# Kernel optimization log

Hardware: AMD Instinct MI355X
Metric: run time of the kernel (lower is better)

Reference implementation:

```python
import jax, jax.numpy as jnp
import numpy as np

N = 50000    # total nodes
F = 32       # raw feature dim
DEG = 32     # padded neighbors per node per relation
B = 2048     # batch nodes
R = 3        # relations


def setup_inputs() -> dict:
    key = jax.random.key(0)
    ks = jax.random.split(key, 12)
    return {
        "nodes": jax.random.randint(ks[0], (B,), 0, N, dtype=jnp.int32),
        "feat_data": jax.random.normal(ks[1], (N, F), dtype=jnp.float32),
        "adj": jax.random.randint(ks[2], (R, N, DEG), 0, N, dtype=jnp.int32),
        "prior": jax.random.uniform(ks[3], (2,), minval=0.1, maxval=0.9, dtype=jnp.float32),
        "w_mlp": jax.random.normal(ks[4], (F, 64), dtype=jnp.float32) * 0.1,
        "b_mlp": jnp.zeros((64,), jnp.float32),
        "alpha1": jax.random.normal(ks[5], (128, R), dtype=jnp.float32) * 0.1,
        "alpha2": jax.random.normal(ks[6], (256, R), dtype=jnp.float32) * 0.1,
        "w_d2": jax.random.normal(ks[7], (448, 2), dtype=jnp.float32) * 0.05,
        "b_d2": jnp.zeros((2,), jnp.float32),
        "w_d1": jax.random.normal(ks[8], (2, 1), dtype=jnp.float32) * 0.5,
        "b_d1": jnp.zeros((1,), jnp.float32),
    }


def _inter_agg(h_all, adj, nodes, alpha, embed_dim):
    """One InterAgg layer. h_all: (N, D) previous-layer features for all nodes;
    adj: (R, N, deg) neighbor ids; nodes: (B,) batch ids; alpha: (2E, R).
    Returns (B, D + 2E)."""
    emb = h_all[:, -embed_dim:]                      # (N, E) last-E slice as in original
    self_full = jnp.take(h_all, nodes, axis=0)       # (B, D)
    self_emb = self_full[:, -embed_dim:]             # (B, E)
    feats = []
    for r in range(R):  # small fixed relation count
        neigh = jnp.take(adj[r], nodes, axis=0)      # (B, deg)
        gathered = jnp.take(emb, neigh.reshape(-1), axis=0)
        agg = gathered.reshape(neigh.shape[0], neigh.shape[1], embed_dim).mean(axis=1)  # masked-mean
        feats.append(jnp.concatenate([agg, self_emb - agg], axis=1))  # IntraAgg concat
    stack = jnp.stack(feats)                         # (R, B, 2E)
    W = jax.nn.softmax(alpha, axis=1)                # (2E, R)
    inter = jnp.einsum('rbe,er->be', stack, W)       # weighted relation combine
    return jnp.concatenate([self_full, inter], axis=1)


def reference(nodes, feat_data, adj, prior, w_mlp, b_mlp, alpha1, alpha2, w_d2, b_d2, w_d1, b_d1):
    # MLP over all nodes (union set == all nodes; per-node values identical)
    h0 = jax.nn.relu(feat_data @ w_mlp + b_mlp)      # (N, 64)
    all_nodes = jnp.arange(h0.shape[0], dtype=jnp.int32)
    h1 = _inter_agg(h0, adj, all_nodes, alpha1, 64)  # (N, 192)
    h2 = _inter_agg(h1, adj, nodes, alpha2, 128)     # (B, 448)
    x = h2 @ w_d2 + b_d2                             # Dense(2)
    x = jax.nn.leaky_relu(x, negative_slope=0.3)
    x = x + jnp.log(prior)
    return jax.nn.sigmoid(x @ w_d1 + b_d1)           # (B, 1)
```

## Files before the change

### kernel.cpp

```cpp
#include <hip/hip_runtime.h>
#include <hip/hip_fp16.h>
#include <math.h>

#define N_NODES 50000
#define F_IN 32
#define DEG 32
#define BATCH 2048
#define NB_STRIDE 100

typedef int int4v __attribute__((ext_vector_type(4)));
typedef unsigned int uint2v __attribute__((ext_vector_type(2)));
typedef float f32x2 __attribute__((ext_vector_type(2)));

__device__ __forceinline__ void softmax3(float a0, float a1, float a2,
                                         float& w0, float& w1, float& w2) {
    float m = fmaxf(a0, fmaxf(a1, a2));
    float e0 = __expf(a0 - m), e1 = __expf(a1 - m), e2 = __expf(a2 - m);
    float s = 1.f / (e0 + e1 + e2);
    w0 = e0 * s; w1 = e1 * s; w2 = e2 * s;
}

__device__ __forceinline__ f32x2 shfl_xor_f2(f32x2 v, int m) {
    v.x = __shfl_xor(v.x, m, 64);
    v.y = __shfl_xor(v.y, m, 64);
    return v;
}

__global__ __launch_bounds__(256) void mlp_kernel(
        const float* __restrict__ feat,
        const float* __restrict__ w,
        const float* __restrict__ b,
        const float* __restrict__ alpha1,
        const float* __restrict__ alpha2,
        float* __restrict__ sw1,
        float* __restrict__ sw2,
        unsigned char* __restrict__ h0q) {
    __shared__ float wl[F_IN * 64];
    __shared__ float fl[8 * F_IN];
    int tid = threadIdx.x;
    if (blockIdx.x == 0) {
        for (int q = tid; q < 384; q += 256) {
            const float* src = (q < 128) ? (alpha1 + q * 3) : (alpha2 + (q - 128) * 3);
            float* dst = (q < 128) ? (sw1 + q * 3) : (sw2 + (q - 128) * 3);
            float w0, w1, w2;
            softmax3(src[0], src[1], src[2], w0, w1, w2);
            dst[0] = w0; dst[1] = w1; dst[2] = w2;
        }
    }
    for (int i = tid; i < F_IN * 64; i += 256) wl[i] = w[i];
    int local = tid >> 5;
    int f2 = (tid & 31) * 2;
    float b0 = b[f2], b1 = b[f2 + 1];
    const int noct = N_NODES / 8;
    for (int q = blockIdx.x; q < noct; q += gridDim.x) {
        int n0 = q * 8;
        __syncthreads();
        fl[tid] = __builtin_nontemporal_load(feat + (size_t)n0 * F_IN + tid);
        __syncthreads();
        float a0 = b0, a1 = b1;
#pragma unroll
        for (int k = 0; k < F_IN; ++k) {
            float v = fl[local * F_IN + k];
            a0 = fmaf(v, wl[k * 64 + f2], a0);
            a1 = fmaf(v, wl[k * 64 + f2 + 1], a1);
        }
        a0 = fmaxf(a0, 0.f);
        a1 = fmaxf(a1, 0.f);
        int n = n0 + local;
        unsigned pk = __builtin_amdgcn_cvt_pk_fp8_f32(a0, a1, 0u, false);
        *reinterpret_cast<unsigned short*>(h0q + (size_t)n * 64 + f2) =
            (unsigned short)pk;
    }
}

__global__ __launch_bounds__(128) void layer1_kernel(
        const int* __restrict__ adj,
        const unsigned char* __restrict__ h0q,
        const float* __restrict__ sw1,
        unsigned char* __restrict__ i1q) {
    __shared__ int nb[16 * NB_STRIDE];
    __shared__ float swl[384];
    int tid = threadIdx.x;
    int n0 = blockIdx.x * 16;
    if (tid < 96)
        reinterpret_cast<float4*>(swl)[tid] = reinterpret_cast<const float4*>(sw1)[tid];
#pragma unroll
    for (int q = tid; q < 384; q += 128) {
        int r = q >> 7;
        int idx = q & 127;
        int m = idx >> 3;
        int d4 = (idx & 7) * 4;
        int4v v = __builtin_nontemporal_load(reinterpret_cast<const int4v*>(
                adj + ((size_t)r * N_NODES + (n0 + m)) * DEG + d4));
        *reinterpret_cast<int4v*>(&nb[m * NB_STRIDE + r * 32 + d4]) = v;
    }
    __syncthreads();
    int w = tid >> 6, j = tid & 63;
    int m = w * 8 + (j >> 3);
    int e = j & 7;
    int n = n0 + m;
    const int* nbrow = nb + m * NB_STRIDE;
    const unsigned char* qb = h0q + 8 * e;
    f32x2 acc0[4] = {}, acc1[4] = {}, acc2[4] = {};
#pragma unroll 8
    for (int t = 0; t < 32; ++t) {
        uint2v d = *reinterpret_cast<const uint2v*>(qb + (size_t)((unsigned)nbrow[t] * 64u));
        acc0[0] += __builtin_amdgcn_cvt_pk_f32_fp8(d.x, false);
        acc0[1] += __builtin_amdgcn_cvt_pk_f32_fp8(d.x, true);
        acc0[2] += __builtin_amdgcn_cvt_pk_f32_fp8(d.y, false);
        acc0[3] += __builtin_amdgcn_cvt_pk_f32_fp8(d.y, true);
    }
#pragma unroll 8
    for (int t = 32; t < 64; ++t) {
        uint2v d = *reinterpret_cast<const uint2v*>(qb + (size_t)((unsigned)nbrow[t] * 64u));
        acc1[0] += __builtin_amdgcn_cvt_pk_f32_fp8(d.x, false);
        acc1[1] += __builtin_amdgcn_cvt_pk_f32_fp8(d.x, true);
        acc1[2] += __builtin_amdgcn_cvt_pk_f32_fp8(d.y, false);
        acc1[3] += __builtin_amdgcn_cvt_pk_f32_fp8(d.y, true);
    }
#pragma unroll 8
    for (int t = 64; t < 96; ++t) {
        uint2v d = *reinterpret_cast<const uint2v*>(qb + (size_t)((unsigned)nbrow[t] * 64u));
        acc2[0] += __builtin_amdgcn_cvt_pk_f32_fp8(d.x, false);
        acc2[1] += __builtin_amdgcn_cvt_pk_f32_fp8(d.x, true);
        acc2[2] += __builtin_amdgcn_cvt_pk_f32_fp8(d.y, false);
        acc2[3] += __builtin_amdgcn_cvt_pk_f32_fp8(d.y, true);
    }

    float sarr[8];
    {
        uint2v sd = *reinterpret_cast<const uint2v*>(qb + (size_t)((unsigned)n * 64u));
        f32x2 s0 = __builtin_amdgcn_cvt_pk_f32_fp8(sd.x, false);
        f32x2 s1 = __builtin_amdgcn_cvt_pk_f32_fp8(sd.x, true);
        f32x2 s2 = __builtin_amdgcn_cvt_pk_f32_fp8(sd.y, false);
        f32x2 s3 = __builtin_amdgcn_cvt_pk_f32_fp8(sd.y, true);
        sarr[0] = s0.x; sarr[1] = s0.y; sarr[2] = s1.x; sarr[3] = s1.y;
        sarr[4] = s2.x; sarr[5] = s2.y; sarr[6] = s3.x; sarr[7] = s3.y;
    }
    float wA[24], wB[24];
    {
        const float4* pa = reinterpret_cast<const float4*>(swl + 24 * e);
        const float4* pb = reinterpret_cast<const float4*>(swl + 192 + 24 * e);
#pragma unroll
        for (int q = 0; q < 6; ++q) {
            float4 ta = pa[q], tb = pb[q];
            wA[4 * q] = ta.x; wA[4 * q + 1] = ta.y; wA[4 * q + 2] = ta.z; wA[4 * q + 3] = ta.w;
            wB[4 * q] = tb.x; wB[4 * q + 1] = tb.y; wB[4 * q + 2] = tb.z; wB[4 * q + 3] = tb.w;
        }
    }
    const float inv = 1.f / 32.f;
    float oa[8], ob[8];
#pragma unroll
    for (int i = 0; i < 8; ++i) {
        float a0 = acc0[i >> 1][i & 1] * inv;
        float a1 = acc1[i >> 1][i & 1] * inv;
        float a2 = acc2[i >> 1][i & 1] * inv;
        float s = sarr[i];
        oa[i] = wA[3 * i] * a0 + wA[3 * i + 1] * a1 + wA[3 * i + 2] * a2;
        ob[i] = wB[3 * i] * (s - a0) + wB[3 * i + 1] * (s - a1) + wB[3 * i + 2] * (s - a2);
    }
    unsigned qa0 = __builtin_amdgcn_cvt_pk_fp8_f32(oa[0], oa[1], 0u, false);
    qa0 = __builtin_amdgcn_cvt_pk_fp8_f32(oa[2], oa[3], qa0, true);
    unsigned qa1 = __builtin_amdgcn_cvt_pk_fp8_f32(oa[4], oa[5], 0u, false);
    qa1 = __builtin_amdgcn_cvt_pk_fp8_f32(oa[6], oa[7], qa1, true);
    uint2v ua = {qa0, qa1};
    __builtin_nontemporal_store(ua,
        reinterpret_cast<uint2v*>(i1q + (size_t)n * 128 + 8 * e));
    unsigned qb0 = __builtin_amdgcn_cvt_pk_fp8_f32(ob[0], ob[1], 0u, false);
    qb0 = __builtin_amdgcn_cvt_pk_fp8_f32(ob[2], ob[3], qb0, true);
    unsigned qb1 = __builtin_amdgcn_cvt_pk_fp8_f32(ob[4], ob[5], 0u, false);
    qb1 = __builtin_amdgcn_cvt_pk_fp8_f32(ob[6], ob[7], qb1, true);
    uint2v ub = {qb0, qb1};
    __builtin_nontemporal_store(ub,
        reinterpret_cast<uint2v*>(i1q + (size_t)n * 128 + 64 + 8 * e));
}

__global__ __launch_bounds__(256) void layer2_kernel(
        const int* __restrict__ nodes,
        const int* __restrict__ adj,
        const unsigned char* __restrict__ h0q,
        const unsigned char* __restrict__ i1q,
        const float* __restrict__ sw2,
        const float* __restrict__ w_d2,
        const float* __restrict__ b_d2,
        const float* __restrict__ w_d1,
        const float* __restrict__ b_d1,
        const float* __restrict__ prior,
        float* __restrict__ out) {
    __shared__ int nb[4][96];
    __shared__ int nid[4];
    __shared__ float swl[768];
    int tid = threadIdx.x;
    int b0 = blockIdx.x * 4;
    if (tid < 4) nid[tid] = nodes[b0 + tid];
    if (tid >= 64 && tid < 256) {
        int q = tid - 64;
        reinterpret_cast<float4*>(swl)[q] = reinterpret_cast<const float4*>(sw2)[q];
    }
    __syncthreads();
    if (tid < 96) {
        int local = tid / 24, rem = tid - local * 24;
        int r = rem >> 3, d4 = (rem & 7) * 4;
        int4v v = __builtin_nontemporal_load(reinterpret_cast<const int4v*>(
                adj + ((size_t)r * N_NODES + nid[local]) * DEG + d4));
        *reinterpret_cast<int4v*>(&nb[local][r * 32 + d4]) = v;
    }
    __syncthreads();
    int local = tid >> 6, j = tid & 63;
    int bb = b0 + local;
    int n = nid[local];
    int g = j >> 4, e = j & 15;
    int idxs[24];
#pragma unroll
    for (int t = 0; t < 24; ++t) idxs[t] = nb[local][t * 4 + g];
    const unsigned char* qbase = i1q + 8 * e;
    f32x2 acc0[4] = {}, acc1[4] = {}, acc2[4] = {};
#pragma unroll
    for (int t = 0; t < 8; ++t) {
        uint2v d = *reinterpret_cast<const uint2v*>(
            qbase + (size_t)((unsigned)idxs[t] * 128u));
        acc0[0] += __builtin_amdgcn_cvt_pk_f32_fp8(d.x, false);
        acc0[1] += __builtin_amdgcn_cvt_pk_f32_fp8(d.x, true);
        acc0[2] += __builtin_amdgcn_cvt_pk_f32_fp8(d.y, false);
        acc0[3] += __builtin_amdgcn_cvt_pk_f32_fp8(d.y, true);
    }
#pragma unroll
    for (int t = 8; t < 16; ++t) {
        uint2v d = *reinterpret_cast<const uint2v*>(
            qbase + (size_t)((unsigned)idxs[t] * 128u));
        acc1[0] += __builtin_amdgcn_cvt_pk_f32_fp8(d.x, false);
        acc1[1] += __builtin_amdgcn_cvt_pk_f32_fp8(d.x, true);
        acc1[2] += __builtin_amdgcn_cvt_pk_f32_fp8(d.y, false);
        acc1[3] += __builtin_amdgcn_cvt_pk_f32_fp8(d.y, true);
    }
#pragma unroll
    for (int t = 16; t < 24; ++t) {
        uint2v d = *reinterpret_cast<const uint2v*>(
            qbase + (size_t)((unsigned)idxs[t] * 128u));
        acc2[0] += __builtin_amdgcn_cvt_pk_f32_fp8(d.x, false);
        acc2[1] += __builtin_amdgcn_cvt_pk_f32_fp8(d.x, true);
        acc2[2] += __builtin_amdgcn_cvt_pk_f32_fp8(d.y, false);
        acc2[3] += __builtin_amdgcn_cvt_pk_f32_fp8(d.y, true);
    }
#pragma unroll
    for (int mm = 16; mm <= 32; mm <<= 1) {
#pragma unroll
        for (int q = 0; q < 4; ++q) {
            acc0[q] += shfl_xor_f2(acc0[q], mm);
            acc1[q] += shfl_xor_f2(acc1[q], mm);
            acc2[q] += shfl_xor_f2(acc2[q], mm);
        }
    }
    const float inv = 1.f / 32.f;
    float p0 = 0.f, p1 = 0.f;
    if (g == 0) {
        float sarr[8];
        {
            uint2v sd = *reinterpret_cast<const uint2v*>(
                qbase + (size_t)((unsigned)n * 128u));
            f32x2 s0 = __builtin_amdgcn_cvt_pk_f32_fp8(sd.x, false);
            f32x2 s1 = __builtin_amdgcn_cvt_pk_f32_fp8(sd.x, true);
            f32x2 s2 = __builtin_amdgcn_cvt_pk_f32_fp8(sd.y, false);
            f32x2 s3 = __builtin_amdgcn_cvt_pk_f32_fp8(sd.y, true);
            sarr[0] = s0.x; sarr[1] = s0.y; sarr[2] = s1.x; sarr[3] = s1.y;
            sarr[4] = s2.x; sarr[5] = s2.y; sarr[6] = s3.x; sarr[7] = s3.y;
        }
        const float* wa = swl + 24 * e;
        const float* wb = swl + 384 + 24 * e;
#pragma unroll
        for (int i = 0; i < 8; ++i) {
            int f = 8 * e + i;
            float a0 = acc0[i >> 1][i & 1] * inv;
            float a1 = acc1[i >> 1][i & 1] * inv;
            float a2 = acc2[i >> 1][i & 1] * inv;
            float s = sarr[i];
            float i2a = wa[3 * i] * a0 + wa[3 * i + 1] * a1 + wa[3 * i + 2] * a2;
            float i2b = wb[3 * i] * (s - a0) + wb[3 * i + 1] * (s - a1) +
                        wb[3 * i + 2] * (s - a2);
            p0 += i2a * w_d2[(192 + f) * 2 + 0] + i2b * w_d2[(320 + f) * 2 + 0];
            p1 += i2a * w_d2[(192 + f) * 2 + 1] + i2b * w_d2[(320 + f) * 2 + 1];
        }
    } else if (g == 1) {
        unsigned d = *reinterpret_cast<const unsigned*>(h0q + (size_t)n * 64 + 4 * e);
        f32x2 lo = __builtin_amdgcn_cvt_pk_f32_fp8(d, false);
        f32x2 hi = __builtin_amdgcn_cvt_pk_f32_fp8(d, true);
        float sv[4] = {lo.x, lo.y, hi.x, hi.y};
#pragma unroll
        for (int i = 0; i < 4; ++i) {
            int f = 4 * e + i;
            p0 += sv[i] * w_d2[f * 2 + 0];
            p1 += sv[i] * w_d2[f * 2 + 1];
        }
    } else if (g == 2) {
        float sarr[8];
        {
            uint2v sd = *reinterpret_cast<const uint2v*>(
                qbase + (size_t)((unsigned)n * 128u));
            f32x2 s0 = __builtin_amdgcn_cvt_pk_f32_fp8(sd.x, false);
            f32x2 s1 = __builtin_amdgcn_cvt_pk_f32_fp8(sd.x, true);
            f32x2 s2 = __builtin_amdgcn_cvt_pk_f32_fp8(sd.y, false);
            f32x2 s3 = __builtin_amdgcn_cvt_pk_f32_fp8(sd.y, true);
            sarr[0] = s0.x; sarr[1] = s0.y; sarr[2] = s1.x; sarr[3] = s1.y;
            sarr[4] = s2.x; sarr[5] = s2.y; sarr[6] = s3.x; sarr[7] = s3.y;
        }
#pragma unroll
        for (int i = 0; i < 8; ++i) {
            int f = 8 * e + i;
            p0 += sarr[i] * w_d2[(64 + f) * 2 + 0];
            p1 += sarr[i] * w_d2[(64 + f) * 2 + 1];
        }
    }
#pragma unroll
    for (int mm = 1; mm <= 32; mm <<= 1) {
        p0 += __shfl_xor(p0, mm, 64);
        p1 += __shfl_xor(p1, mm, 64);
    }
    if (j == 0) {
        float x0 = p0 + b_d2[0], x1 = p1 + b_d2[1];
        x0 = x0 > 0.f ? x0 : 0.3f * x0;
        x1 = x1 > 0.f ? x1 : 0.3f * x1;
        x0 += __logf(prior[0]);
        x1 += __logf(prior[1]);
        float z = x0 * w_d1[0] + x1 * w_d1[1] + b_d1[0];
        out[bb] = 1.f / (1.f + __expf(-z));
    }
}

extern "C" void kernel_launch(void* const* d_in, const int* in_sizes, int n_in,
                              void* d_out, int out_size, void* d_ws, size_t ws_size,
                              hipStream_t stream) {
    const int*   nodes  = (const int*)d_in[0];
    const float* feat   = (const float*)d_in[1];
    const int*   adj    = (const int*)d_in[2];
    const float* prior  = (const float*)d_in[3];
    const float* w_mlp  = (const float*)d_in[4];
    const float* b_mlp  = (const float*)d_in[5];
    const float* alpha1 = (const float*)d_in[6];
    const float* alpha2 = (const float*)d_in[7];
    const float* w_d2   = (const float*)d_in[8];
    const float* b_d2   = (const float*)d_in[9];
    const float* w_d1   = (const float*)d_in[10];
    const float* b_d1   = (const float*)d_in[11];
    float* out = (float*)d_out;

    float* sw1 = (float*)d_ws;
    float* sw2 = sw1 + 128 * 3;
    unsigned char* h0q = (unsigned char*)((char*)d_ws + 8192);
    unsigned char* i1q = h0q + (size_t)N_NODES * 64;

    mlp_kernel<<<2048, 256, 0, stream>>>(feat, w_mlp, b_mlp, alpha1, alpha2,
                                         sw1, sw2, h0q);
    layer1_kernel<<<N_NODES / 16, 128, 0, stream>>>(adj, h0q, sw1, i1q);
    layer2_kernel<<<BATCH / 4, 256, 0, stream>>>(nodes, adj, h0q, i1q, sw2,
                                                 w_d2, b_d2, w_d1, b_d1, prior, out);
}
```

Measured before the change: 55.26 us.

## Split layer1 neighbor loop across 4 lanes with 16-byte gathers and shuffle reduce

Layer1 now runs 256 threads per block. Each node's 64-dim fp8 row is covered by 4 lanes doing 16-byte loads, and the 32 neighbors per relation are split across 4 lane groups whose partial sums are combined with xor shuffles. The relation weights are stored transposed in shared memory so they can be read as float4 vectors. The aim is more memory-level parallelism and wider loads in the gather-bound step, at the cost of extra shuffles and more registers for the accumulators.

```diff
diff --git a/kernel.cpp b/kernel.cpp
--- a/kernel.cpp
+++ b/kernel.cpp
@@ -10,7 +10,9 @@
 
 typedef int int4v __attribute__((ext_vector_type(4)));
 typedef unsigned int uint2v __attribute__((ext_vector_type(2)));
+typedef unsigned int uint4v __attribute__((ext_vector_type(4)));
 typedef float f32x2 __attribute__((ext_vector_type(2)));
+typedef float f32x4 __attribute__((ext_vector_type(4)));
 
 __device__ __forceinline__ void softmax3(float a0, float a1, float a2,
                                          float& w0, float& w1, float& w2) {
@@ -73,21 +75,22 @@
     }
 }
 
-__global__ __launch_bounds__(128) void layer1_kernel(
+__global__ __launch_bounds__(256) void layer1_kernel(
         const int* __restrict__ adj,
         const unsigned char* __restrict__ h0q,
         const float* __restrict__ sw1,
         unsigned char* __restrict__ i1q) {
     __shared__ int nb[16 * NB_STRIDE];
-    __shared__ float swl[384];
+    __shared__ alignas(16) float swlT[6][64];
     int tid = threadIdx.x;
     int n0 = blockIdx.x * 16;
-    if (tid < 96)
-        reinterpret_cast<float4*>(swl)[tid] = reinterpret_cast<const float4*>(sw1)[tid];
-#pragma unroll
-    for (int q = tid; q < 384; q += 128) {
-        int r = q >> 7;
-        int idx = q & 127;
+    for (int t = tid; t < 384; t += 256) {
+        int p = t >> 6, f = t & 63;
+        swlT[p][f] = (p < 3) ? sw1[f * 3 + p] : sw1[(64 + f) * 3 + (p - 3)];
+    }
+    for (int t = tid; t < 384; t += 256) {
+        int r = t >> 7;
+        int idx = t & 127;
         int m = idx >> 3;
         int d4 = (idx & 7) * 4;
         int4v v = __builtin_nontemporal_load(reinterpret_cast<const int4v*>(
@@ -96,83 +99,104 @@
     }
     __syncthreads();
     int w = tid >> 6, j = tid & 63;
-    int m = w * 8 + (j >> 3);
-    int e = j & 7;
-    int n = n0 + m;
-    const int* nbrow = nb + m * NB_STRIDE;
-    const unsigned char* qb = h0q + 8 * e;
-    f32x2 acc0[4] = {}, acc1[4] = {}, acc2[4] = {};
-#pragma unroll 8
-    for (int t = 0; t < 32; ++t) {
-        uint2v d = *reinterpret_cast<const uint2v*>(qb + (size_t)((unsigned)nbrow[t] * 64u));
+    int m = j >> 4;
+    int q = j & 3;
+    int rg = (j >> 2) & 3;
+    int nodeLocal = w * 4 + m;
+    int n = n0 + nodeLocal;
+    const int* nbrow = nb + nodeLocal * NB_STRIDE;
+    const unsigned char* qb = h0q + 16 * q;
+    f32x2 acc0[8] = {}, acc1[8] = {}, acc2[8] = {};
+#pragma unroll
+    for (int t = 0; t < 8; ++t) {
+        unsigned row = (unsigned)nbrow[rg + 4 * t];
+        uint4v d = *reinterpret_cast<const uint4v*>(qb + (size_t)(row * 64u));
         acc0[0] += __builtin_amdgcn_cvt_pk_f32_fp8(d.x, false);
         acc0[1] += __builtin_amdgcn_cvt_pk_f32_fp8(d.x, true);
         acc0[2] += __builtin_amdgcn_cvt_pk_f32_fp8(d.y, false);
         acc0[3] += __builtin_amdgcn_cvt_pk_f32_fp8(d.y, true);
-    }
-#pragma unroll 8
-    for (int t = 32; t < 64; ++t) {
-        uint2v d = *reinterpret_cast<const uint2v*>(qb + (size_t)((unsigned)nbrow[t] * 64u));
+        acc0[4] += __builtin_amdgcn_cvt_pk_f32_fp8(d.z, false);
+        acc0[5] += __builtin_amdgcn_cvt_pk_f32_fp8(d.z, true);
+        acc0[6] += __builtin_amdgcn_cvt_pk_f32_fp8(d.w, false);
+        acc0[7] += __builtin_amdgcn_cvt_pk_f32_fp8(d.w, true);
+    }
+#pragma unroll
+    for (int t = 0; t < 8; ++t) {
+        unsigned row = (unsigned)nbrow[32 + rg + 4 * t];
+        uint4v d = *reinterpret_cast<const uint4v*>(qb + (size_t)(row * 64u));
         acc1[0] += __builtin_amdgcn_cvt_pk_f32_fp8(d.x, false);
         acc1[1] += __builtin_amdgcn_cvt_pk_f32_fp8(d.x, true);
         acc1[2] += __builtin_amdgcn_cvt_pk_f32_fp8(d.y, false);
         acc1[3] += __builtin_amdgcn_cvt_pk_f32_fp8(d.y, true);
-    }
-#pragma unroll 8
-    for (int t = 64; t < 96; ++t) {
-        uint2v d = *reinterpret_cast<const uint2v*>(qb + (size_t)((unsigned)nbrow[t] * 64u));
+        acc1[4] += __builtin_amdgcn_cvt_pk_f32_fp8(d.z, false);
+        acc1[5] += __builtin_amdgcn_cvt_pk_f32_fp8(d.z, true);
+        acc1[6] += __builtin_amdgcn_cvt_pk_f32_fp8(d.w, false);
+        acc1[7] += __builtin_amdgcn_cvt_pk_f32_fp8(d.w, true);
+    }
+#pragma unroll
+    for (int t = 0; t < 8; ++t) {
+        unsigned row = (unsigned)nbrow[64 + rg + 4 * t];
+        uint4v d = *reinterpret_cast<const uint4v*>(qb + (size_t)(row * 64u));
         acc2[0] += __builtin_amdgcn_cvt_pk_f32_fp8(d.x, false);
         acc2[1] += __builtin_amdgcn_cvt_pk_f32_fp8(d.x, true);
         acc2[2] += __builtin_amdgcn_cvt_pk_f32_fp8(d.y, false);
         acc2[3] += __builtin_amdgcn_cvt_pk_f32_fp8(d.y, true);
-    }
-
-    float sarr[8];
-    {
-        uint2v sd = *reinterpret_cast<const uint2v*>(qb + (size_t)((unsigned)n * 64u));
-        f32x2 s0 = __builtin_amdgcn_cvt_pk_f32_fp8(sd.x, false);
-        f32x2 s1 = __builtin_amdgcn_cvt_pk_f32_fp8(sd.x, true);
-        f32x2 s2 = __builtin_amdgcn_cvt_pk_f32_fp8(sd.y, false);
-        f32x2 s3 = __builtin_amdgcn_cvt_pk_f32_fp8(sd.y, true);
-        sarr[0] = s0.x; sarr[1] = s0.y; sarr[2] = s1.x; sarr[3] = s1.y;
-        sarr[4] = s2.x; sarr[5] = s2.y; sarr[6] = s3.x; sarr[7] = s3.y;
-    }
-    float wA[24], wB[24];
-    {
-        const float4* pa = reinterpret_cast<const float4*>(swl + 24 * e);
-        const float4* pb = reinterpret_cast<const float4*>(swl + 192 + 24 * e);
-#pragma unroll
-        for (int q = 0; q < 6; ++q) {
-            float4 ta = pa[q], tb = pb[q];
-            wA[4 * q] = ta.x; wA[4 * q + 1] = ta.y; wA[4 * q + 2] = ta.z; wA[4 * q + 3] = ta.w;
-            wB[4 * q] = tb.x; wB[4 * q + 1] = tb.y; wB[4 * q + 2] = tb.z; wB[4 * q + 3] = tb.w;
-        }
-    }
+        acc2[4] += __builtin_amdgcn_cvt_pk_f32_fp8(d.z, false);
+        acc2[5] += __builtin_amdgcn_cvt_pk_f32_fp8(d.z, true);
+        acc2[6] += __builtin_amdgcn_cvt_pk_f32_fp8(d.w, false);
+        acc2[7] += __builtin_amdgcn_cvt_pk_f32_fp8(d.w, true);
+    }
+#pragma unroll
+    for (int mm = 4; mm <= 8; mm <<= 1) {
+#pragma unroll
+        for (int k = 0; k < 8; ++k) {
+            acc0[k] += shfl_xor_f2(acc0[k], mm);
+            acc1[k] += shfl_xor_f2(acc1[k], mm);
+            acc2[k] += shfl_xor_f2(acc2[k], mm);
+        }
+    }
+    uint4v sd = *reinterpret_cast<const uint4v*>(qb + (size_t)((unsigned)n * 64u));
+    unsigned sdw[4] = {sd.x, sd.y, sd.z, sd.w};
     const float inv = 1.f / 32.f;
-    float oa[8], ob[8];
-#pragma unroll
-    for (int i = 0; i < 8; ++i) {
-        float a0 = acc0[i >> 1][i & 1] * inv;
-        float a1 = acc1[i >> 1][i & 1] * inv;
-        float a2 = acc2[i >> 1][i & 1] * inv;
-        float s = sarr[i];
-        oa[i] = wA[3 * i] * a0 + wA[3 * i + 1] * a1 + wA[3 * i + 2] * a2;
-        ob[i] = wB[3 * i] * (s - a0) + wB[3 * i + 1] * (s - a1) + wB[3 * i + 2] * (s - a2);
-    }
-    unsigned qa0 = __builtin_amdgcn_cvt_pk_fp8_f32(oa[0], oa[1], 0u, false);
-    qa0 = __builtin_amdgcn_cvt_pk_fp8_f32(oa[2], oa[3], qa0, true);
-    unsigned qa1 = __builtin_amdgcn_cvt_pk_fp8_f32(oa[4], oa[5], 0u, false);
-    qa1 = __builtin_amdgcn_cvt_pk_fp8_f32(oa[6], oa[7], qa1, true);
-    uint2v ua = {qa0, qa1};
-    __builtin_nontemporal_store(ua,
-        reinterpret_cast<uint2v*>(i1q + (size_t)n * 128 + 8 * e));
-    unsigned qb0 = __builtin_amdgcn_cvt_pk_fp8_f32(ob[0], ob[1], 0u, false);
-    qb0 = __builtin_amdgcn_cvt_pk_fp8_f32(ob[2], ob[3], qb0, true);
-    unsigned qb1 = __builtin_amdgcn_cvt_pk_fp8_f32(ob[4], ob[5], 0u, false);
-    qb1 = __builtin_amdgcn_cvt_pk_fp8_f32(ob[6], ob[7], qb1, true);
-    uint2v ub = {qb0, qb1};
-    __builtin_nontemporal_store(ub,
-        reinterpret_cast<uint2v*>(i1q + (size_t)n * 128 + 64 + 8 * e));
+    uint4v ua, ub;
+    unsigned uaw[4], ubw[4];
+#pragma unroll
+    for (int c = 0; c < 4; ++c) {
+        int fb = 16 * q + 4 * c;
+        f32x4 wa0 = *reinterpret_cast<const f32x4*>(&swlT[0][fb]);
+        f32x4 wa1 = *reinterpret_cast<const f32x4*>(&swlT[1][fb]);
+        f32x4 wa2 = *reinterpret_cast<const f32x4*>(&swlT[2][fb]);
+        f32x4 wb0 = *reinterpret_cast<const f32x4*>(&swlT[3][fb]);
+        f32x4 wb1 = *reinterpret_cast<const f32x4*>(&swlT[4][fb]);
+        f32x4 wb2 = *reinterpret_cast<const f32x4*>(&swlT[5][fb]);
+        f32x2 slo = __builtin_amdgcn_cvt_pk_f32_fp8(sdw[c], false);
+        f32x2 shi = __builtin_amdgcn_cvt_pk_f32_fp8(sdw[c], true);
+        float sv[4] = {slo.x, slo.y, shi.x, shi.y};
+        float oa[4], ob[4];
+#pragma unroll
+        for (int k = 0; k < 4; ++k) {
+            int i = 4 * c + k;
+            float a0 = acc0[i >> 1][i & 1] * inv;
+            float a1 = acc1[i >> 1][i & 1] * inv;
+            float a2 = acc2[i >> 1][i & 1] * inv;
+            float s = sv[k];
+            oa[k] = wa0[k] * a0 + wa1[k] * a1 + wa2[k] * a2;
+            ob[k] = wb0[k] * (s - a0) + wb1[k] * (s - a1) + wb2[k] * (s - a2);
+        }
+        unsigned u = __builtin_amdgcn_cvt_pk_fp8_f32(oa[0], oa[1], 0u, false);
+        uaw[c] = __builtin_amdgcn_cvt_pk_fp8_f32(oa[2], oa[3], u, true);
+        u = __builtin_amdgcn_cvt_pk_fp8_f32(ob[0], ob[1], 0u, false);
+        ubw[c] = __builtin_amdgcn_cvt_pk_fp8_f32(ob[2], ob[3], u, true);
+    }
+    ua.x = uaw[0]; ua.y = uaw[1]; ua.z = uaw[2]; ua.w = uaw[3];
+    ub.x = ubw[0]; ub.y = ubw[1]; ub.z = ubw[2]; ub.w = ubw[3];
+    if (rg == 0) {
+        __builtin_nontemporal_store(ua,
+            reinterpret_cast<uint4v*>(i1q + (size_t)n * 128 + 16 * q));
+    } else if (rg == 1) {
+        __builtin_nontemporal_store(ub,
+            reinterpret_cast<uint4v*>(i1q + (size_t)n * 128 + 64 + 16 * q));
+    }
 }
 
 __global__ __launch_bounds__(256) void layer2_kernel(
@@ -350,7 +374,7 @@
 
     mlp_kernel<<<2048, 256, 0, stream>>>(feat, w_mlp, b_mlp, alpha1, alpha2,
                                          sw1, sw2, h0q);
-    layer1_kernel<<<N_NODES / 16, 128, 0, stream>>>(adj, h0q, sw1, i1q);
+    layer1_kernel<<<N_NODES / 16, 256, 0, stream>>>(adj, h0q, sw1, i1q);
     layer2_kernel<<<BATCH / 4, 256, 0, stream>>>(nodes, adj, h0q, i1q, sw2,
                                                  w_d2, b_d2, w_d1, b_d1, prior, out);
 }
```

New measurement: 60.46 us. 1.09x slower.
